# Kernel tuning notes

Hardware: AMD Instinct MI355X
Metric: run time of the kernel (lower is better)

The kernel has to match this reference:

```python
import jax, jax.numpy as jnp
import numpy as np

B, V, T, S, C, NH, H, MULT = 1, 2, 2, 16384, 128, 9, 4, 2
DH = C // H


def _ln(x, g, b):
    m = jnp.mean(x, -1, keepdims=True)
    v = jnp.mean((x - m) ** 2, -1, keepdims=True)
    return (x - m) * jax.lax.rsqrt(v + 1e-5) * g + b


def setup_inputs():
    key = jax.random.key(0)
    ks = jax.random.split(key, 16)
    sc = 0.02
    return {
        "x": jax.random.normal(ks[0], (B, V, T, S, C), jnp.float32),
        "adjc": jax.random.randint(ks[1], (S, NH), 0, S, dtype=jnp.int32),
        "mask": jax.random.bernoulli(ks[2], 0.1, (B, V, T, S)),
        "ln1_g": jnp.ones((C,), jnp.float32),
        "ln1_b": jnp.zeros((C,), jnp.float32),
        "Wq": sc * jax.random.normal(ks[3], (C, C), jnp.float32),
        "Wkv": sc * jax.random.normal(ks[4], (C, 2 * C), jnp.float32),
        "b_kv": jnp.zeros((2 * C,), jnp.float32),
        "W_nh": sc * jax.random.normal(ks[5], (NH, NH), jnp.float32),
        "W_ao": sc * jax.random.normal(ks[6], (C, C), jnp.float32),
        "ln2_g": jnp.ones((C,), jnp.float32),
        "ln2_b": jnp.zeros((C,), jnp.float32),
        "W1": sc * jax.random.normal(ks[7], (C, MULT * C), jnp.float32),
        "b1": jnp.zeros((MULT * C,), jnp.float32),
        "W2": sc * jax.random.normal(ks[8], (MULT * C, C), jnp.float32),
        "b2": jnp.zeros((C,), jnp.float32),
        "gamma": 0.1 * jnp.ones((C,), jnp.float32),
        "Wout": sc * jax.random.normal(ks[9], (C, C), jnp.float32),
    }


def reference(x, adjc, mask, ln1_g, ln1_b, Wq, Wkv, b_kv, W_nh, W_ao,
              ln2_g, ln2_b, W1, b1, W2, b2, gamma, Wout):
    # 1. per-zoom embedding layer (LayerNorm, identity linear)
    xe = _ln(x, ln1_g, ln1_b)  # [b,v,t,s,c]
    # 2. query projection, q_len = 1 per grid cell
    q = jnp.einsum("bvtsc,cd->bvtsd", xe, Wq)
    # 3. neighborhood gather (grid_layer.get_nh) + fused KV projection
    kv_nh = xe[:, :, :, adjc, :]                       # [b,v,t,s,nh,c]
    kv = jnp.einsum("bvtsnc,cd->bvtsnd", kv_nh, Wkv) + b_kv  # [b,v,t,s,nh,2c]
    # factorized nh-mixing with residual skip (skip_dims=[True,...])
    kv = kv + jnp.einsum("bvtsnd,nm->bvtsmd", kv, W_nh)
    # 4. gathered neighbor mask (True = masked out)
    m_nh = mask[:, :, :, adjc]                          # [b,v,t,s,nh]
    # 5. multi-head cross attention, q_len=1, kv_len=nh
    k, v = jnp.split(kv, 2, axis=-1)                    # each [b,v,t,s,nh,c]
    qh = q.reshape(B, V, T, S, H, DH)
    kh = k.reshape(B, V, T, S, NH, H, DH)
    vh = v.reshape(B, V, T, S, NH, H, DH)
    scores = jnp.einsum("bvtshd,bvtsnhd->bvtshn", qh, kh) / jnp.sqrt(
        jnp.asarray(DH, qh.dtype))
    scores = jnp.where(m_nh[:, :, :, :, None, :], -1e9, scores)
    attn = jax.nn.softmax(scores, axis=-1)
    o = jnp.einsum("bvtshn,bvtsnhd->bvtshd", attn, vh).reshape(B, V, T, S, C)
    o = jnp.einsum("bvtsc,cd->bvtsd", o, W_ao)
    # 6. residual insert
    x = x + o
    # 7. MLP block with layer-scale gamma
    xm = _ln(x, ln2_g, ln2_b)
    h = jax.nn.gelu(jnp.einsum("bvtsc,cd->bvtsd", xm, W1) + b1)
    x = x + gamma * (jnp.einsum("bvtsd,dc->bvtsc", h, W2) + b2)
    # 8. output layer
    return jnp.einsum("bvtsc,cd->bvtsd", x, Wout)
```

## Files before the change

### kernel.cpp

```cpp
#include <hip/hip_runtime.h>
#include <math.h>

namespace {

typedef float f32x4 __attribute__((ext_vector_type(4)));
typedef short s16x8 __attribute__((ext_vector_type(8)));

constexpr int C_   = 128;
constexpr int S_   = 16384;
constexpr int NTOK = 65536;

__device__ __forceinline__ unsigned short f2bf(float f) {
    unsigned int u = __float_as_uint(f);
    unsigned int r = (u + 0x7FFFu + ((u >> 16) & 1u)) >> 16;
    return (unsigned short)r;
}
__device__ __forceinline__ float bf2f(unsigned short h) {
    return __uint_as_float(((unsigned int)h) << 16);
}
__device__ __forceinline__ float gelu_tanh(float v) {
    const float k0 = 0.7978845608028654f;
    float u = k0 * (v + 0.044715f * v * v * v);
    float au = fabsf(u);
    float E = __expf(2.0f * au);
    float th = 1.0f - 2.0f / (1.0f + E);
    th = (u < 0.f) ? -th : th;
    return 0.5f * v * (1.0f + th);
}

__global__ __launch_bounds__(256) void prep_weights(
    const float* __restrict__ Wq, const float* __restrict__ Wkv,
    const float* __restrict__ W_ao, const float* __restrict__ W1,
    const float* __restrict__ W2, const float* __restrict__ Wout,
    unsigned short* __restrict__ Wf)
{
    int idx = blockIdx.x * 256 + threadIdx.x;
    if (idx >= 147456) return;
    int seg, off, K, N; const float* src = nullptr;
    if (idx < 49152)       { seg = 0; off = 0;      K = 128; N = 384; }
    else if (idx < 65536)  { seg = 1; off = 49152;  K = 128; N = 128; src = W_ao; }
    else if (idx < 98304)  { seg = 2; off = 65536;  K = 128; N = 256; src = W1; }
    else if (idx < 131072) { seg = 3; off = 98304;  K = 256; N = 128; src = W2; }
    else                   { seg = 4; off = 131072; K = 128; N = 128; src = Wout; }
    int local = idx - off;
    int j    = local & 7;
    int lane = (local >> 3) & 63;
    int tl   = local >> 9;
    int KB   = K >> 5;
    int kb   = tl % KB;
    int nt   = tl / KB;
    int k    = kb * 32 + ((lane >> 4) << 3) + j;
    int col  = (nt << 4) + (lane & 15);
    float v;
    if (seg == 0) v = (col < 128) ? Wq[k * 128 + col] : Wkv[k * 256 + (col - 128)];
    else          v = src[k * N + col];
    Wf[idx] = f2bf(v);
}

__global__ __launch_bounds__(256, 2) void qkv_kernel(
    const float* __restrict__ x,
    const float* __restrict__ ln1_g, const float* __restrict__ ln1_b,
    const unsigned short* __restrict__ Wf,
    const float* __restrict__ b_kv,
    float* qout, unsigned short* __restrict__ kout,
    unsigned short* __restrict__ vout)
{
    __shared__ unsigned short xet[64 * 128];
    const int tile = blockIdx.x;
    const int t = threadIdx.x;

    {
        const int row = t >> 2;
        const int q4  = t & 3;
        const int tok = tile * 64 + row;
        const float* xr = x + (size_t)tok * C_ + q4 * 32;
        float v[32];
        float s0 = 0.f, s1 = 0.f;
        #pragma unroll
        for (int i = 0; i < 32; i += 4) {
            float4 f = *(const float4*)(xr + i);
            v[i] = f.x; v[i+1] = f.y; v[i+2] = f.z; v[i+3] = f.w;
            s0 += f.x + f.y + f.z + f.w;
            s1 += f.x*f.x + f.y*f.y + f.z*f.z + f.w*f.w;
        }
        s0 += __shfl_xor(s0, 1, 64); s1 += __shfl_xor(s1, 1, 64);
        s0 += __shfl_xor(s0, 2, 64); s1 += __shfl_xor(s1, 2, 64);
        const float mean = s0 * (1.0f / C_);
        const float var  = s1 * (1.0f / C_) - mean * mean;
        const float inv  = rsqrtf(var + 1e-5f);
        #pragma unroll
        for (int jj = 0; jj < 4; ++jj) {
            unsigned short tmp[8];
            #pragma unroll
            for (int j = 0; j < 8; ++j) {
                int k = q4 * 32 + jj * 8 + j;
                tmp[j] = f2bf((v[jj*8 + j] - mean) * inv * ln1_g[k] + ln1_b[k]);
            }
            int byte = row * 256 + (q4 * 32 + jj * 8) * 2;
            byte ^= (row & 7) << 4;
            *(s16x8*)((char*)xet + byte) = *(const s16x8*)tmp;
        }
    }
    __syncthreads();

    const int w = t >> 6, l = t & 63;
    const int arow = (w << 4) + (l & 15);
    s16x8 af[4];
    #pragma unroll
    for (int kb = 0; kb < 4; ++kb) {
        int byte = arow * 256 + (kb * 32 + ((l >> 4) << 3)) * 2;
        byte ^= (arow & 7) << 4;
        af[kb] = *(const s16x8*)((const char*)xet + byte);
    }
    f32x4 acc[24];
    #pragma unroll
    for (int nt = 0; nt < 24; ++nt) acc[nt] = (f32x4){0.f, 0.f, 0.f, 0.f};
    #pragma unroll
    for (int nt = 0; nt < 24; ++nt) {
        #pragma unroll
        for (int kb = 0; kb < 4; ++kb) {
            s16x8 bf = *(const s16x8*)(Wf + (size_t)((nt * 4 + kb) * 64 + l) * 8);
            acc[nt] = __builtin_amdgcn_mfma_f32_16x16x32_bf16(af[kb], bf, acc[nt], 0, 0, 0);
        }
    }
    const int r0 = (l >> 4) << 2;
    const int colb = l & 15;
    #pragma unroll
    for (int nt = 0; nt < 8; ++nt) {
        const int col = nt * 16 + colb;
        #pragma unroll
        for (int reg = 0; reg < 4; ++reg) {
            const size_t tokr = (size_t)tile * 64 + (w << 4) + r0 + reg;
            qout[tokr * 128 + col] = acc[nt][reg];
        }
    }
    #pragma unroll
    for (int i = 0; i < 8; ++i) {
        const int ch = i * 16 + colb;
        const float bk = b_kv[ch];
        const float bv = b_kv[ch + 128];
        #pragma unroll
        for (int reg = 0; reg < 4; ++reg) {
            const size_t tokr = (size_t)tile * 64 + (w << 4) + r0 + reg;
            kout[tokr * 128 + ch] = f2bf(acc[8 + i][reg] + bk);
            vout[tokr * 128 + ch] = f2bf(acc[16 + i][reg] + bv);
        }
    }
}

__global__ __launch_bounds__(256, 2) void attn_mlp_kernel(
    const float* __restrict__ x,
    const int* __restrict__ adjc, const unsigned char* __restrict__ mask,
    const float* __restrict__ wnh,
    const float* __restrict__ qbuf,
    const unsigned short* __restrict__ kbuf,
    const unsigned short* __restrict__ vbuf,
    const unsigned short* __restrict__ Wao_f, const unsigned short* __restrict__ W1f,
    const unsigned short* __restrict__ W2f, const unsigned short* __restrict__ Woutf,
    const float* __restrict__ ln2_g, const float* __restrict__ ln2_b,
    const float* __restrict__ b1, const float* __restrict__ b2,
    const float* __restrict__ gamma,
    float* outp)
{
    __shared__ unsigned short act[8192];
    __shared__ float sred[2][32][2];
    __shared__ unsigned int sidx[32][9];

    const int d   = blockIdx.x;
    const int xcd = d & 7, dj = d >> 3;
    const int bid = (xcd >> 1) * 512 + dj * 2 + (xcd & 1);
    const size_t base = (size_t)bid * 32;
    const int s0  = (int)(base & (S_ - 1));
    const int bvt = (int)(base >> 14);
    const int t = threadIdx.x;

    for (int i = t; i < 288; i += 256) {
        int r = i / 9, n = i - r * 9;
        int nb = adjc[(s0 + r) * 9 + n];
        unsigned int gi = (unsigned int)(bvt * S_ + nb);
        sidx[r][n] = gi | (mask[gi] ? 0x80000000u : 0u);
    }
    __syncthreads();

    {
        const int r = t >> 3, j = t & 7;
        const size_t tok = base + r;

        float q[16];
        {
            const float4* qp = (const float4*)(qbuf + tok * 128 + j * 16);
            #pragma unroll
            for (int i = 0; i < 4; ++i) {
                float4 f = qp[i];
                q[4*i] = f.x; q[4*i+1] = f.y; q[4*i+2] = f.z; q[4*i+3] = f.w;
            }
        }
        unsigned int gm[9];
        #pragma unroll
        for (int n = 0; n < 9; ++n) gm[n] = sidx[r][n];

        float sp[9];
        #pragma unroll
        for (int n = 0; n < 9; ++n) {
            const s16x8* kp = (const s16x8*)(kbuf +
                (size_t)(gm[n] & 0x7fffffffu) * 128 + j * 16);
            s16x8 k0 = kp[0], k1 = kp[1];
            float a = 0.f;
            #pragma unroll
            for (int i = 0; i < 8; ++i) a += q[i]     * bf2f((unsigned short)k0[i]);
            #pragma unroll
            for (int i = 0; i < 8; ++i) a += q[8 + i] * bf2f((unsigned short)k1[i]);
            sp[n] = a;
        }
        #pragma unroll
        for (int n = 0; n < 9; ++n) sp[n] += __shfl_xor(sp[n], 1, 64);

        float S[9];
        #pragma unroll
        for (int m = 0; m < 9; ++m) {
            float a = sp[m];
            #pragma unroll
            for (int n = 0; n < 9; ++n) a += sp[n] * wnh[n * 9 + m];
            a *= 0.17677669529663687f;
            S[m] = (gm[m] & 0x80000000u) ? -1e9f : a;
        }
        float mx = S[0];
        #pragma unroll
        for (int m = 1; m < 9; ++m) mx = fmaxf(mx, S[m]);
        float e[9], se = 0.f;
        #pragma unroll
        for (int m = 0; m < 9; ++m) { e[m] = __expf(S[m] - mx); se += e[m]; }
        const float inv = 1.f / se;

        float ap[9];
        #pragma unroll
        for (int n = 0; n < 9; ++n) {
            float a = e[n];
            #pragma unroll
            for (int m = 0; m < 9; ++m) a += wnh[n * 9 + m] * e[m];
            ap[n] = a * inv;
        }

        float o[16];
        #pragma unroll
        for (int i = 0; i < 16; ++i) o[i] = 0.f;
        #pragma unroll
        for (int n = 0; n < 9; ++n) {
            const s16x8* vp = (const s16x8*)(vbuf +
                (size_t)(gm[n] & 0x7fffffffu) * 128 + j * 16);
            s16x8 v0 = vp[0], v1 = vp[1];
            const float a = ap[n];
            #pragma unroll
            for (int i = 0; i < 8; ++i) o[i]     += a * bf2f((unsigned short)v0[i]);
            #pragma unroll
            for (int i = 0; i < 8; ++i) o[8 + i] += a * bf2f((unsigned short)v1[i]);
        }
        unsigned short tmp[16];
        #pragma unroll
        for (int i = 0; i < 16; ++i) tmp[i] = f2bf(o[i]);
        int b0 = (r * 256 + j * 32) ^ ((r & 7) << 4);
        int b1_ = (r * 256 + j * 32 + 16) ^ ((r & 7) << 4);
        *(s16x8*)((char*)act + b0)  = *(const s16x8*)tmp;
        *(s16x8*)((char*)act + b1_) = *(const s16x8*)(tmp + 8);
    }
    __syncthreads();

    const int w = t >> 6, l = t & 63;
    const int wr = w >> 1, wc = w & 1;
    const int arow = (wr << 4) + (l & 15);
    const int crow0 = (wr << 4) + ((l >> 4) << 2);
    const int colb = l & 15;

    s16x8 af[4];
    #pragma unroll
    for (int kb = 0; kb < 4; ++kb) {
        int byte = arow * 256 + (kb * 32 + ((l >> 4) << 3)) * 2;
        byte ^= (arow & 7) << 4;
        af[kb] = *(const s16x8*)((const char*)act + byte);
    }
    f32x4 acc1[4];
    #pragma unroll
    for (int nt = 0; nt < 4; ++nt) acc1[nt] = (f32x4){0.f, 0.f, 0.f, 0.f};
    #pragma unroll
    for (int nt = 0; nt < 4; ++nt) {
        const int ntg = wc * 4 + nt;
        #pragma unroll
        for (int kb = 0; kb < 4; ++kb) {
            s16x8 bf = *(const s16x8*)(Wao_f + (size_t)((ntg * 4 + kb) * 64 + l) * 8);
            acc1[nt] = __builtin_amdgcn_mfma_f32_16x16x32_bf16(af[kb], bf, acc1[nt], 0, 0, 0);
        }
    }

    float x1v[4][4];
    float ss[4] = {0.f, 0.f, 0.f, 0.f}, s2[4] = {0.f, 0.f, 0.f, 0.f};
    #pragma unroll
    for (int nt = 0; nt < 4; ++nt) {
        const int col = wc * 64 + nt * 16 + colb;
        #pragma unroll
        for (int reg = 0; reg < 4; ++reg) {
            const size_t tokr = base + crow0 + reg;
            float xv = x[tokr * 128 + col] + acc1[nt][reg];
            x1v[nt][reg] = xv;
            ss[reg] += xv;
            s2[reg] += xv * xv;
        }
    }
    #pragma unroll
    for (int off = 1; off < 16; off <<= 1) {
        #pragma unroll
        for (int reg = 0; reg < 4; ++reg) {
            ss[reg] += __shfl_xor(ss[reg], off, 64);
            s2[reg] += __shfl_xor(s2[reg], off, 64);
        }
    }
    if (colb == 0) {
        #pragma unroll
        for (int reg = 0; reg < 4; ++reg) {
            sred[wc][crow0 + reg][0] = ss[reg];
            sred[wc][crow0 + reg][1] = s2[reg];
        }
    }
    __syncthreads();
    float mean[4], inv[4];
    #pragma unroll
    for (int reg = 0; reg < 4; ++reg) {
        const int row = crow0 + reg;
        float sum = sred[0][row][0] + sred[1][row][0];
        float sq  = sred[0][row][1] + sred[1][row][1];
        mean[reg] = sum * (1.0f / 128.f);
        float var = sq * (1.0f / 128.f) - mean[reg] * mean[reg];
        inv[reg] = rsqrtf(var + 1e-5f);
    }
    __syncthreads();
    #pragma unroll
    for (int nt = 0; nt < 4; ++nt) {
        const int col = wc * 64 + nt * 16 + colb;
        const float lg = ln2_g[col], lb = ln2_b[col];
        #pragma unroll
        for (int reg = 0; reg < 4; ++reg) {
            const int lrow = crow0 + reg;
            float xm = (x1v[nt][reg] - mean[reg]) * inv[reg] * lg + lb;
            int byte = lrow * 256 + col * 2;
            byte ^= (lrow & 7) << 4;
            *(unsigned short*)((char*)act + byte) = f2bf(xm);
        }
    }
    __syncthreads();

    #pragma unroll
    for (int kb = 0; kb < 4; ++kb) {
        int byte = arow * 256 + (kb * 32 + ((l >> 4) << 3)) * 2;
        byte ^= (arow & 7) << 4;
        af[kb] = *(const s16x8*)((const char*)act + byte);
    }
    f32x4 acc2[8];
    #pragma unroll
    for (int nt = 0; nt < 8; ++nt) acc2[nt] = (f32x4){0.f, 0.f, 0.f, 0.f};
    #pragma unroll
    for (int nt = 0; nt < 8; ++nt) {
        const int ntg = wc * 8 + nt;
        #pragma unroll
        for (int kb = 0; kb < 4; ++kb) {
            s16x8 bf = *(const s16x8*)(W1f + (size_t)((ntg * 4 + kb) * 64 + l) * 8);
            acc2[nt] = __builtin_amdgcn_mfma_f32_16x16x32_bf16(af[kb], bf, acc2[nt], 0, 0, 0);
        }
    }
    __syncthreads();
    #pragma unroll
    for (int nt = 0; nt < 8; ++nt) {
        const int col2 = wc * 128 + nt * 16 + colb;
        const float bb = b1[col2];
        #pragma unroll
        for (int reg = 0; reg < 4; ++reg) {
            const int lrow = crow0 + reg;
            float hv = gelu_tanh(acc2[nt][reg] + bb);
            int byte = lrow * 512 + col2 * 2;
            byte ^= (lrow & 7) << 4;
            *(unsigned short*)((char*)act + byte) = f2bf(hv);
        }
    }
    __syncthreads();

    f32x4 acc3[4];
    #pragma unroll
    for (int nt = 0; nt < 4; ++nt) acc3[nt] = (f32x4){0.f, 0.f, 0.f, 0.f};
    #pragma unroll
    for (int kb = 0; kb < 8; ++kb) {
        int byte = arow * 512 + (kb * 32 + ((l >> 4) << 3)) * 2;
        byte ^= (arow & 7) << 4;
        s16x8 hf = *(const s16x8*)((const char*)act + byte);
        #pragma unroll
        for (int nt = 0; nt < 4; ++nt) {
            const int ntg = wc * 4 + nt;
            s16x8 bf = *(const s16x8*)(W2f + (size_t)((ntg * 8 + kb) * 64 + l) * 8);
            acc3[nt] = __builtin_amdgcn_mfma_f32_16x16x32_bf16(hf, bf, acc3[nt], 0, 0, 0);
        }
    }
    __syncthreads();
    #pragma unroll
    for (int nt = 0; nt < 4; ++nt) {
        const int col = wc * 64 + nt * 16 + colb;
        const float gm = gamma[col], bb = b2[col];
        #pragma unroll
        for (int reg = 0; reg < 4; ++reg) {
            const int lrow = crow0 + reg;
            float y = x1v[nt][reg] + gm * (acc3[nt][reg] + bb);
            int byte = lrow * 256 + col * 2;
            byte ^= (lrow & 7) << 4;
            *(unsigned short*)((char*)act + byte) = f2bf(y);
        }
    }
    __syncthreads();

    #pragma unroll
    for (int kb = 0; kb < 4; ++kb) {
        int byte = arow * 256 + (kb * 32 + ((l >> 4) << 3)) * 2;
        byte ^= (arow & 7) << 4;
        af[kb] = *(const s16x8*)((const char*)act + byte);
    }
    f32x4 acc4[4];
    #pragma unroll
    for (int nt = 0; nt < 4; ++nt) acc4[nt] = (f32x4){0.f, 0.f, 0.f, 0.f};
    #pragma unroll
    for (int nt = 0; nt < 4; ++nt) {
        const int ntg = wc * 4 + nt;
        #pragma unroll
        for (int kb = 0; kb < 4; ++kb) {
            s16x8 bf = *(const s16x8*)(Woutf + (size_t)((ntg * 4 + kb) * 64 + l) * 8);
            acc4[nt] = __builtin_amdgcn_mfma_f32_16x16x32_bf16(af[kb], bf, acc4[nt], 0, 0, 0);
        }
    }
    #pragma unroll
    for (int nt = 0; nt < 4; ++nt) {
        const int col = wc * 64 + nt * 16 + colb;
        #pragma unroll
        for (int reg = 0; reg < 4; ++reg) {
            const size_t tokr = base + crow0 + reg;
            outp[tokr * 128 + col] = acc4[nt][reg];
        }
    }
}

}

extern "C" void kernel_launch(void* const* d_in, const int* in_sizes, int n_in,
                              void* d_out, int out_size, void* d_ws, size_t ws_size,
                              hipStream_t stream) {
    const float* x     = (const float*)d_in[0];
    const int*   adjc  = (const int*)d_in[1];
    const unsigned char* mask = (const unsigned char*)d_in[2];
    const float* ln1_g = (const float*)d_in[3];
    const float* ln1_b = (const float*)d_in[4];
    const float* Wq    = (const float*)d_in[5];
    const float* Wkv   = (const float*)d_in[6];
    const float* b_kv  = (const float*)d_in[7];
    const float* W_nh  = (const float*)d_in[8];
    const float* W_ao  = (const float*)d_in[9];
    const float* ln2_g = (const float*)d_in[10];
    const float* ln2_b = (const float*)d_in[11];
    const float* W1    = (const float*)d_in[12];
    const float* b1    = (const float*)d_in[13];
    const float* W2    = (const float*)d_in[14];
    const float* b2    = (const float*)d_in[15];
    const float* gamma = (const float*)d_in[16];
    const float* Wout  = (const float*)d_in[17];

    unsigned short* kbuf = (unsigned short*)d_ws;
    unsigned short* vbuf = kbuf + (size_t)NTOK * 128;
    unsigned short* Wf   = vbuf + (size_t)NTOK * 128;
    unsigned short* Wao_f  = Wf + 49152;
    unsigned short* W1f    = Wf + 65536;
    unsigned short* W2f    = Wf + 98304;
    unsigned short* Woutf  = Wf + 131072;

    float* qbuf = (float*)d_out;

    prep_weights<<<576, 256, 0, stream>>>(Wq, Wkv, W_ao, W1, W2, Wout, Wf);
    qkv_kernel<<<NTOK / 64, 256, 0, stream>>>(x, ln1_g, ln1_b, Wf, b_kv,
                                              qbuf, kbuf, vbuf);
    attn_mlp_kernel<<<NTOK / 32, 256, 0, stream>>>(x, adjc, mask, W_nh,
                                                   qbuf, kbuf, vbuf,
                                                   Wao_f, W1f, W2f, Woutf,
                                                   ln2_g, ln2_b, b1, b2, gamma,
                                                   (float*)d_out);
}
```

Before: 134.2 us.

## Store K/V in FP8 e4m3 and retile QKV kernel to 32-token blocks

K and V projections are now stored as FP8 e4m3 bytes instead of bf16, halving the bytes written by the QKV kernel and the bytes gathered per neighbour in the attention kernel. The QKV kernel is also retiled to 32 tokens per block, with waves split across output-column halves and twice as many blocks launched. The cost is extra decode work per element in the attention inner loops and lower precision for K and V, which may exceed accuracy tolerance.

Measured after the change: 172.1 us. 1.28x slower.

```diff
diff --git a/kernel.cpp b/kernel.cpp
--- a/kernel.cpp
+++ b/kernel.cpp
@@ -1,10 +1,12 @@
 #include <hip/hip_runtime.h>
+#include <hip/hip_fp8.h>
 #include <math.h>
 
 namespace {
 
 typedef float f32x4 __attribute__((ext_vector_type(4)));
 typedef short s16x8 __attribute__((ext_vector_type(8)));
+typedef unsigned int u32x4 __attribute__((ext_vector_type(4)));
 
 constexpr int C_   = 128;
 constexpr int S_   = 16384;
@@ -17,6 +19,14 @@
 }
 __device__ __forceinline__ float bf2f(unsigned short h) {
     return __uint_as_float(((unsigned int)h) << 16);
+}
+__device__ __forceinline__ unsigned char ftofp8(float f) {
+    __hip_fp8_e4m3 t(f);
+    return t.__x;
+}
+__device__ __forceinline__ float fp8tof(unsigned char b) {
+    __hip_fp8_e4m3 t; t.__x = b;
+    return (float)t;
 }
 __device__ __forceinline__ float gelu_tanh(float v) {
     const float k0 = 0.7978845608028654f;
@@ -62,22 +72,22 @@
     const float* __restrict__ ln1_g, const float* __restrict__ ln1_b,
     const unsigned short* __restrict__ Wf,
     const float* __restrict__ b_kv,
-    float* qout, unsigned short* __restrict__ kout,
-    unsigned short* __restrict__ vout)
+    float* qout, unsigned char* __restrict__ kout,
+    unsigned char* __restrict__ vout)
 {
-    __shared__ unsigned short xet[64 * 128];
+    __shared__ unsigned short xet[32 * 128];
     const int tile = blockIdx.x;
     const int t = threadIdx.x;
 
     {
-        const int row = t >> 2;
-        const int q4  = t & 3;
-        const int tok = tile * 64 + row;
-        const float* xr = x + (size_t)tok * C_ + q4 * 32;
-        float v[32];
+        const int row = t >> 3;
+        const int j   = t & 7;
+        const int tok = tile * 32 + row;
+        const float* xr = x + (size_t)tok * C_ + j * 16;
+        float v[16];
         float s0 = 0.f, s1 = 0.f;
         #pragma unroll
-        for (int i = 0; i < 32; i += 4) {
+        for (int i = 0; i < 16; i += 4) {
             float4 f = *(const float4*)(xr + i);
             v[i] = f.x; v[i+1] = f.y; v[i+2] = f.z; v[i+3] = f.w;
             s0 += f.x + f.y + f.z + f.w;
@@ -85,26 +95,26 @@
         }
         s0 += __shfl_xor(s0, 1, 64); s1 += __shfl_xor(s1, 1, 64);
         s0 += __shfl_xor(s0, 2, 64); s1 += __shfl_xor(s1, 2, 64);
+        s0 += __shfl_xor(s0, 4, 64); s1 += __shfl_xor(s1, 4, 64);
         const float mean = s0 * (1.0f / C_);
         const float var  = s1 * (1.0f / C_) - mean * mean;
         const float inv  = rsqrtf(var + 1e-5f);
-        #pragma unroll
-        for (int jj = 0; jj < 4; ++jj) {
-            unsigned short tmp[8];
-            #pragma unroll
-            for (int j = 0; j < 8; ++j) {
-                int k = q4 * 32 + jj * 8 + j;
-                tmp[j] = f2bf((v[jj*8 + j] - mean) * inv * ln1_g[k] + ln1_b[k]);
-            }
-            int byte = row * 256 + (q4 * 32 + jj * 8) * 2;
-            byte ^= (row & 7) << 4;
-            *(s16x8*)((char*)xet + byte) = *(const s16x8*)tmp;
-        }
+        unsigned short tmp[16];
+        #pragma unroll
+        for (int i = 0; i < 16; ++i) {
+            int c = j * 16 + i;
+            tmp[i] = f2bf((v[i] - mean) * inv * ln1_g[c] + ln1_b[c]);
+        }
+        int b0 = (row * 256 + j * 32) ^ ((row & 7) << 4);
+        int b1_ = (row * 256 + j * 32 + 16) ^ ((row & 7) << 4);
+        *(s16x8*)((char*)xet + b0)  = *(const s16x8*)tmp;
+        *(s16x8*)((char*)xet + b1_) = *(const s16x8*)(tmp + 8);
     }
     __syncthreads();
 
     const int w = t >> 6, l = t & 63;
-    const int arow = (w << 4) + (l & 15);
+    const int wr = w >> 1, wc = w & 1;
+    const int arow = (wr << 4) + (l & 15);
     s16x8 af[4];
     #pragma unroll
     for (int kb = 0; kb < 4; ++kb) {
@@ -112,38 +122,36 @@
         byte ^= (arow & 7) << 4;
         af[kb] = *(const s16x8*)((const char*)xet + byte);
     }
-    f32x4 acc[24];
-    #pragma unroll
-    for (int nt = 0; nt < 24; ++nt) acc[nt] = (f32x4){0.f, 0.f, 0.f, 0.f};
-    #pragma unroll
-    for (int nt = 0; nt < 24; ++nt) {
+    f32x4 acc[12];
+    #pragma unroll
+    for (int nt = 0; nt < 12; ++nt) acc[nt] = (f32x4){0.f, 0.f, 0.f, 0.f};
+    #pragma unroll
+    for (int nt = 0; nt < 12; ++nt) {
+        const int ntg = wc * 12 + nt;
         #pragma unroll
         for (int kb = 0; kb < 4; ++kb) {
-            s16x8 bf = *(const s16x8*)(Wf + (size_t)((nt * 4 + kb) * 64 + l) * 8);
+            s16x8 bf = *(const s16x8*)(Wf + (size_t)((ntg * 4 + kb) * 64 + l) * 8);
             acc[nt] = __builtin_amdgcn_mfma_f32_16x16x32_bf16(af[kb], bf, acc[nt], 0, 0, 0);
         }
     }
-    const int r0 = (l >> 4) << 2;
+    const int crow0 = (wr << 4) + ((l >> 4) << 2);
     const int colb = l & 15;
     #pragma unroll
-    for (int nt = 0; nt < 8; ++nt) {
-        const int col = nt * 16 + colb;
-        #pragma unroll
-        for (int reg = 0; reg < 4; ++reg) {
-            const size_t tokr = (size_t)tile * 64 + (w << 4) + r0 + reg;
-            qout[tokr * 128 + col] = acc[nt][reg];
-        }
-    }
-    #pragma unroll
-    for (int i = 0; i < 8; ++i) {
-        const int ch = i * 16 + colb;
-        const float bk = b_kv[ch];
-        const float bv = b_kv[ch + 128];
-        #pragma unroll
-        for (int reg = 0; reg < 4; ++reg) {
-            const size_t tokr = (size_t)tile * 64 + (w << 4) + r0 + reg;
-            kout[tokr * 128 + ch] = f2bf(acc[8 + i][reg] + bk);
-            vout[tokr * 128 + ch] = f2bf(acc[16 + i][reg] + bv);
+    for (int nt = 0; nt < 12; ++nt) {
+        const int gcol = (wc * 12 + nt) * 16 + colb;
+        #pragma unroll
+        for (int reg = 0; reg < 4; ++reg) {
+            const size_t tokr = (size_t)tile * 32 + crow0 + reg;
+            const float val = acc[nt][reg];
+            if (gcol < 128) {
+                qout[tokr * 128 + gcol] = val;
+            } else if (gcol < 256) {
+                const int ch = gcol - 128;
+                kout[tokr * 128 + ch] = ftofp8(val + b_kv[ch]);
+            } else {
+                const int ch = gcol - 256;
+                vout[tokr * 128 + ch] = ftofp8(val + b_kv[ch + 128]);
+            }
         }
     }
 }
@@ -153,8 +161,8 @@
     const int* __restrict__ adjc, const unsigned char* __restrict__ mask,
     const float* __restrict__ wnh,
     const float* __restrict__ qbuf,
-    const unsigned short* __restrict__ kbuf,
-    const unsigned short* __restrict__ vbuf,
+    const unsigned char* __restrict__ kbuf,
+    const unsigned char* __restrict__ vbuf,
     const unsigned short* __restrict__ Wao_f, const unsigned short* __restrict__ W1f,
     const unsigned short* __restrict__ W2f, const unsigned short* __restrict__ Woutf,
     const float* __restrict__ ln2_g, const float* __restrict__ ln2_b,
@@ -202,14 +210,17 @@
         float sp[9];
         #pragma unroll
         for (int n = 0; n < 9; ++n) {
-            const s16x8* kp = (const s16x8*)(kbuf +
+            u32x4 kq = *(const u32x4*)(kbuf +
                 (size_t)(gm[n] & 0x7fffffffu) * 128 + j * 16);
-            s16x8 k0 = kp[0], k1 = kp[1];
             float a = 0.f;
             #pragma unroll
-            for (int i = 0; i < 8; ++i) a += q[i]     * bf2f((unsigned short)k0[i]);
-            #pragma unroll
-            for (int i = 0; i < 8; ++i) a += q[8 + i] * bf2f((unsigned short)k1[i]);
+            for (int wi = 0; wi < 4; ++wi) {
+                unsigned int u = kq[wi];
+                a += q[4*wi]     * fp8tof((unsigned char)(u & 0xffu));
+                a += q[4*wi + 1] * fp8tof((unsigned char)((u >> 8) & 0xffu));
+                a += q[4*wi + 2] * fp8tof((unsigned char)((u >> 16) & 0xffu));
+                a += q[4*wi + 3] * fp8tof((unsigned char)(u >> 24));
+            }
             sp[n] = a;
         }
         #pragma unroll
@@ -246,14 +257,17 @@
         for (int i = 0; i < 16; ++i) o[i] = 0.f;
         #pragma unroll
         for (int n = 0; n < 9; ++n) {
-            const s16x8* vp = (const s16x8*)(vbuf +
+            u32x4 vq = *(const u32x4*)(vbuf +
                 (size_t)(gm[n] & 0x7fffffffu) * 128 + j * 16);
-            s16x8 v0 = vp[0], v1 = vp[1];
             const float a = ap[n];
             #pragma unroll
-            for (int i = 0; i < 8; ++i) o[i]     += a * bf2f((unsigned short)v0[i]);
-            #pragma unroll
-            for (int i = 0; i < 8; ++i) o[8 + i] += a * bf2f((unsigned short)v1[i]);
+            for (int wi = 0; wi < 4; ++wi) {
+                unsigned int u = vq[wi];
+                o[4*wi]     += a * fp8tof((unsigned char)(u & 0xffu));
+                o[4*wi + 1] += a * fp8tof((unsigned char)((u >> 8) & 0xffu));
+                o[4*wi + 2] += a * fp8tof((unsigned char)((u >> 16) & 0xffu));
+                o[4*wi + 3] += a * fp8tof((unsigned char)(u >> 24));
+            }
         }
         unsigned short tmp[16];
         #pragma unroll
@@ -465,9 +479,9 @@
     const float* gamma = (const float*)d_in[16];
     const float* Wout  = (const float*)d_in[17];
 
-    unsigned short* kbuf = (unsigned short*)d_ws;
-    unsigned short* vbuf = kbuf + (size_t)NTOK * 128;
-    unsigned short* Wf   = vbuf + (size_t)NTOK * 128;
+    unsigned char* kbuf = (unsigned char*)d_ws;
+    unsigned char* vbuf = kbuf + (size_t)NTOK * 128;
+    unsigned short* Wf  = (unsigned short*)(vbuf + (size_t)NTOK * 128);
     unsigned short* Wao_f  = Wf + 49152;
     unsigned short* W1f    = Wf + 65536;
     unsigned short* W2f    = Wf + 98304;
@@ -476,7 +490,7 @@
     float* qbuf = (float*)d_out;
 
     prep_weights<<<576, 256, 0, stream>>>(Wq, Wkv, W_ao, W1, W2, Wout, Wf);
-    qkv_kernel<<<NTOK / 64, 256, 0, stream>>>(x, ln1_g, ln1_b, Wf, b_kv,
+    qkv_kernel<<<NTOK / 32, 256, 0, stream>>>(x, ln1_g, ln1_b, Wf, b_kv,
                                               qbuf, kbuf, vbuf);
     attn_mlp_kernel<<<NTOK / 32, 256, 0, stream>>>(x, adjc, mask, W_nh,
                                                    qbuf, kbuf, vbuf,
```
